# Performance work log

Hardware: AMD Instinct MI355X
Metric: run time of the kernel (lower is better)

The kernel has to match this reference:

```python
import jax, jax.numpy as jnp
import numpy as np

HIDDEN = 768
FFN = 3072
E = 8
TOP_K = 2


def setup_inputs() -> dict:
    key = jax.random.key(0)
    k_x, k_r, k_w1, k_w2 = jax.random.split(key, 4)
    x = jax.random.normal(k_x, (1, 1024, HIDDEN), dtype=jnp.float32)
    # nn.Linear(hidden, E, bias=False): weight applied as x @ W^T; store as [H, E]
    bound = 1.0 / np.sqrt(HIDDEN)
    router_w = jax.random.uniform(k_r, (HIDDEN, E), minval=-bound, maxval=bound, dtype=jnp.float32)
    w1 = jax.random.normal(k_w1, (E, HIDDEN, FFN), dtype=jnp.float32) * 0.02
    w2 = jax.random.normal(k_w2, (E, FFN, HIDDEN), dtype=jnp.float32) * 0.02
    return {"x": x, "router_w": router_w, "w1": w1, "w2": w2}


def reference(x, router_w, w1, w2):
    B, T, H = x.shape
    xf = x.reshape(-1, H)                                  # [N, H]
    logits = xf @ router_w                                 # [N, E] (eval mode: no noise)
    probs = jax.nn.softmax(logits, axis=-1)
    top_v, top_i = jax.lax.top_k(probs, TOP_K)             # [N, K]
    top_v = top_v / jnp.sum(top_v, axis=-1, keepdims=True)  # renormalize top-k probs
    # Combine top-k weights into a dense per-expert gate; zero gates make the
    # dense per-expert computation mathematically identical to sparse dispatch.
    gates = jnp.sum(jax.nn.one_hot(top_i, E, dtype=xf.dtype) * top_v[..., None], axis=1)  # [N, E]
    h = jax.nn.gelu(jnp.einsum('nh,ehf->enf', xf, w1), approximate=False)  # [E, N, F]
    y = jnp.einsum('enf,efh->enh', h, w2)                  # [E, N, H]
    out = jnp.einsum('ne,enh->nh', gates, y)               # [N, H]
    return out.reshape(B, T, H)
```

## Files before the change

kernel.cpp:

```cpp
#include <hip/hip_runtime.h>
#include <cmath>

#define NTOK 1024
#define HD   768
#define FF   3072
#define NE   8
#define NSLOT (NTOK * 2)
#define BK   64
#define CLD  130
#define NB_CONV 4608

typedef unsigned short u16;
typedef unsigned int   u32;
typedef __bf16 bf16x8 __attribute__((ext_vector_type(8)));
typedef float  f32x4  __attribute__((ext_vector_type(4)));
typedef u16    u16x8  __attribute__((ext_vector_type(8)));

__device__ __forceinline__ u16 f2bf(float f) {
  union { float f; u32 u; } v; v.f = f;
  u32 r = v.u + 0x7FFFu + ((v.u >> 16) & 1u);
  return (u16)(r >> 16);
}

__device__ __forceinline__ void load16(const void* g, void* l) {
  __builtin_amdgcn_global_load_lds(
      (const __attribute__((address_space(1))) u32*)g,
      (__attribute__((address_space(3))) u32*)l, 16, 0, 0);
}

__global__ __launch_bounds__(256) void convert_router_kernel(
    const float* __restrict__ w1, const float* __restrict__ w2,
    u16* __restrict__ w1t, u16* __restrict__ w2t,
    const float* __restrict__ x, const float* __restrict__ rw,
    u16* __restrict__ xb, int* __restrict__ counts,
    int* __restrict__ ti, int* __restrict__ tpos, float* __restrict__ tg)
{
  __shared__ char smem[NE * HD * 4];
  const int tid  = threadIdx.x;
  const int lane = tid & 63;
  const int wid  = tid >> 6;

  if (blockIdx.x < NB_CONV) {
    const int z   = blockIdx.x / 288;
    const int rem = blockIdx.x % 288;
    const float* src; u16* dst; int K, N, n0, k0;
    if (z < NE) {
      src = w1 + (size_t)z * HD * FF;  dst = w1t + (size_t)z * FF * HD;
      K = HD; N = FF;
      n0 = (rem % 48) * 64;  k0 = (rem / 48) * 128;
    } else {
      src = w2 + (size_t)(z - NE) * FF * HD;  dst = w2t + (size_t)(z - NE) * HD * FF;
      K = FF; N = HD;
      k0 = (rem % 24) * 128; n0 = (rem / 24) * 64;
    }
    u16* lt = (u16*)smem;
    const int rr = tid >> 4;
    const int cc = (tid & 15) << 2;
#pragma unroll
    for (int j = 0; j < 8; ++j) {
      const int k = j * 16 + rr;
      const float4 v = *(const float4*)(src + (size_t)(k0 + k) * N + n0 + cc);
      lt[(cc + 0) * CLD + k] = f2bf(v.x); lt[(cc + 1) * CLD + k] = f2bf(v.y);
      lt[(cc + 2) * CLD + k] = f2bf(v.z); lt[(cc + 3) * CLD + k] = f2bf(v.w);
    }
    __syncthreads();
    const int l15 = lane & 15;
    const int r4  = lane >> 4;
#pragma unroll
    for (int s = 0; s < 4; ++s) {
      const int r = wid * 16 + s * 4 + r4;
      u16x8 v;
#pragma unroll
      for (int d = 0; d < 8; ++d) v[d] = lt[r * CLD + l15 * 8 + d];
      *(u16x8*)(dst + (size_t)(n0 + r) * K + k0 + l15 * 8) = v;
    }
  } else {
    float* rwt = (float*)smem;
    for (int i = tid; i < NE * HD; i += 256) {
      const int h = i >> 3, e = i & 7;
      rwt[e * HD + h] = rw[i];
    }
    __syncthreads();

    const int t = (blockIdx.x - NB_CONV) * 4 + wid;
    const float* xrow = x + (size_t)t * HD;
    u16* xbrow = xb + (size_t)t * HD;

    float acc[NE] = {};
#pragma unroll
    for (int j = 0; j < 12; ++j) {
      const int h = lane + j * 64;
      const float xv = xrow[h];
      xbrow[h] = f2bf(xv);
#pragma unroll
      for (int e = 0; e < NE; ++e) acc[e] += xv * rwt[e * HD + h];
    }
#pragma unroll
    for (int e = 0; e < NE; ++e) {
      float v = acc[e];
#pragma unroll
      for (int off = 32; off; off >>= 1) v += __shfl_down(v, off, 64);
      acc[e] = v;
    }

    if (lane == 0) {
      float v0 = -1e30f, v1 = -1e30f; int i0 = 0, i1 = 0;
#pragma unroll
      for (int e = 0; e < NE; ++e) {
        const float p = acc[e];
        if (p > v0) { v1 = v0; i1 = i0; v0 = p; i0 = e; }
        else if (p > v1) { v1 = p; i1 = e; }
      }
      const float e1 = expf(v1 - v0);
      const float g0 = 1.0f / (1.0f + e1);
      const float g1 = e1 / (1.0f + e1);
      const int p0 = atomicAdd(&counts[i0], 1);
      const int p1 = atomicAdd(&counts[i1], 1);
      ti[2 * t] = i0;  ti[2 * t + 1] = i1;
      tpos[2 * t] = p0; tpos[2 * t + 1] = p1;
      tg[2 * t] = g0;  tg[2 * t + 1] = g1;
    }
  }
}

__global__ __launch_bounds__(1024) void router_scatter(
    const int* __restrict__ counts, const int* __restrict__ ti,
    const int* __restrict__ tpos, const float* __restrict__ tg,
    int* __restrict__ tos, float* __restrict__ gos, int* __restrict__ seg)
{
  __shared__ int offs[NE];
  const int t = threadIdx.x;
  if (t == 0) {
    int o = 0;
    for (int e = 0; e < NE; ++e) {
      offs[e] = o; seg[e] = o; seg[NE + e] = counts[e]; o += counts[e];
    }
  }
  __syncthreads();
  const int i0 = ti[2 * t], i1 = ti[2 * t + 1];
  const int s0 = offs[i0] + tpos[2 * t];
  const int s1 = offs[i1] + tpos[2 * t + 1];
  tos[s0] = t; gos[s0] = tg[2 * t];
  tos[s1] = t; gos[s1] = tg[2 * t + 1];
}


__global__ __launch_bounds__(256) void ffn1_kernel(
    const u16* __restrict__ xb, const u16* __restrict__ w1t,
    const int* __restrict__ tos, const int* __restrict__ seg,
    u16* __restrict__ hbuf)
{
  const int e   = blockIdx.z;
  const int cnt = seg[NE + e];
  const int m0  = blockIdx.y * 128;
  if (m0 >= cnt) return;
  const int start = seg[e];
  const int n0    = blockIdx.x * 64;

  __shared__ __align__(16) u16 As[128 * 64];
  __shared__ __align__(16) u16 Bs[64 * 64];
  __shared__ int toks[128];

  const int tid = threadIdx.x;
  if (tid < 128) toks[tid] = tos[start + min(m0 + tid, cnt - 1)];
  __syncthreads();

  const int lane = tid & 63;
  const int wid  = tid >> 6;
  const int rsub = lane >> 3;
  const int c8   = (lane & 7) ^ rsub;

  const u16* ag[4]; u16* al[4];
#pragma unroll
  for (int i = 0; i < 4; ++i) {
    const int rb = wid * 8 + i * 32;
    ag[i] = xb + (size_t)toks[rb + rsub] * HD + c8 * 8;
    al[i] = As + rb * 64;
  }
  const u16* bg[2]; u16* bl[2];
#pragma unroll
  for (int i = 0; i < 2; ++i) {
    const int rb = wid * 8 + i * 32;
    bg[i] = w1t + ((size_t)e * FF + n0 + rb + rsub) * HD + c8 * 8;
    bl[i] = Bs + rb * 64;
  }

  const int wm  = (wid >> 1) << 6;
  const int wn  = (wid & 1) << 5;
  const int q   = lane >> 4;
  const int r16 = lane & 15;

  f32x4 acc[4][2] = {};

  for (int k0 = 0; k0 < HD; k0 += BK) {
#pragma unroll
    for (int i = 0; i < 4; ++i) load16(ag[i] + k0, al[i]);
#pragma unroll
    for (int i = 0; i < 2; ++i) load16(bg[i] + k0, bl[i]);
    __syncthreads();
#pragma unroll
    for (int s = 0; s < 2; ++s) {
      const int pa = ((s << 2) + q) ^ (r16 & 7);
      bf16x8 af[4], bf[2];
#pragma unroll
      for (int t = 0; t < 4; ++t)
        af[t] = *(const bf16x8*)(&As[(wm + t * 16 + r16) * 64 + pa * 8]);
#pragma unroll
      for (int t = 0; t < 2; ++t)
        bf[t] = *(const bf16x8*)(&Bs[(wn + t * 16 + r16) * 64 + pa * 8]);
#pragma unroll
      for (int t = 0; t < 4; ++t)
#pragma unroll
        for (int c = 0; c < 2; ++c)
          acc[t][c] = __builtin_amdgcn_mfma_f32_16x16x32_bf16(af[t], bf[c], acc[t][c], 0, 0, 0);
    }
    __syncthreads();
  }

#pragma unroll
  for (int t = 0; t < 4; ++t) {
    const int mbase = m0 + wm + t * 16 + q * 4;
#pragma unroll
    for (int i = 0; i < 4; ++i) {
      if (mbase + i < cnt) {
        u16* drow = hbuf + (size_t)(start + mbase + i) * FF + n0 + wn;
#pragma unroll
        for (int c = 0; c < 2; ++c) {
          float v = acc[t][c][i];
          v = 0.5f * v * (1.0f + erff(v * 0.70710678118f));
          drow[c * 16 + r16] = f2bf(v);
        }
      }
    }
  }
}

#define KSPLIT 4
#define KSEG   (FF / KSPLIT)

__global__ __launch_bounds__(256) void ffn2_kernel(
    const u16* __restrict__ hbuf, const u16* __restrict__ w2t,
    const int* __restrict__ tos, const float* __restrict__ gos,
    const int* __restrict__ seg, float* __restrict__ out)
{
  const int ez  = blockIdx.z;
  const int e   = ez >> 2;
  const int ks  = ez & 3;
  const int cnt = seg[NE + e];
  const int m0  = blockIdx.y * 128;
  if (m0 >= cnt) return;
  const int start = seg[e];
  const int n0    = blockIdx.x * 64;
  const int kbase = ks * KSEG;

  __shared__ __align__(16) u16 As[128 * 64];
  __shared__ __align__(16) u16 Bs[64 * 64];
  __shared__ int   toks[128];
  __shared__ float gates[128];

  const int tid = threadIdx.x;
  if (tid < 128) {
    const int idx = start + min(m0 + tid, cnt - 1);
    toks[tid]  = tos[idx];
    gates[tid] = gos[idx];
  }
  __syncthreads();

  const int lane = tid & 63;
  const int wid  = tid >> 6;
  const int rsub = lane >> 3;
  const int c8   = (lane & 7) ^ rsub;

  const u16* ag[4]; u16* al[4];
#pragma unroll
  for (int i = 0; i < 4; ++i) {
    const int rb = wid * 8 + i * 32;
    ag[i] = hbuf + (size_t)(start + min(m0 + rb + rsub, cnt - 1)) * FF + kbase + c8 * 8;
    al[i] = As + rb * 64;
  }
  const u16* bg[2]; u16* bl[2];
#pragma unroll
  for (int i = 0; i < 2; ++i) {
    const int rb = wid * 8 + i * 32;
    bg[i] = w2t + ((size_t)e * HD + n0 + rb + rsub) * FF + kbase + c8 * 8;
    bl[i] = Bs + rb * 64;
  }

  const int wm  = (wid >> 1) << 6;
  const int wn  = (wid & 1) << 5;
  const int q   = lane >> 4;
  const int r16 = lane & 15;

  f32x4 acc[4][2] = {};

  for (int k0 = 0; k0 < KSEG; k0 += BK) {
#pragma unroll
    for (int i = 0; i < 4; ++i) load16(ag[i] + k0, al[i]);
#pragma unroll
    for (int i = 0; i < 2; ++i) load16(bg[i] + k0, bl[i]);
    __syncthreads();
#pragma unroll
    for (int s = 0; s < 2; ++s) {
      const int pa = ((s << 2) + q) ^ (r16 & 7);
      bf16x8 af[4], bf[2];
#pragma unroll
      for (int t = 0; t < 4; ++t)
        af[t] = *(const bf16x8*)(&As[(wm + t * 16 + r16) * 64 + pa * 8]);
#pragma unroll
      for (int t = 0; t < 2; ++t)
        bf[t] = *(const bf16x8*)(&Bs[(wn + t * 16 + r16) * 64 + pa * 8]);
#pragma unroll
      for (int t = 0; t < 4; ++t)
#pragma unroll
        for (int c = 0; c < 2; ++c)
          acc[t][c] = __builtin_amdgcn_mfma_f32_16x16x32_bf16(af[t], bf[c], acc[t][c], 0, 0, 0);
    }
    __syncthreads();
  }

#pragma unroll
  for (int t = 0; t < 4; ++t) {
    const int mbase = wm + t * 16 + q * 4;
#pragma unroll
    for (int i = 0; i < 4; ++i) {
      const int mloc = mbase + i;
      if (m0 + mloc < cnt) {
        const int tok  = toks[mloc];
        const float g  = gates[mloc];
        float* drow = out + (size_t)tok * HD + n0 + wn;
#pragma unroll
        for (int c = 0; c < 2; ++c) {
          atomicAdd(drow + c * 16 + r16, g * acc[t][c][i]);
        }
      }
    }
  }
}

extern "C" void kernel_launch(void* const* d_in, const int* in_sizes, int n_in,
                              void* d_out, int out_size, void* d_ws, size_t ws_size,
                              hipStream_t stream) {
  const float* x  = (const float*)d_in[0];
  const float* rw = (const float*)d_in[1];
  const float* w1 = (const float*)d_in[2];
  const float* w2 = (const float*)d_in[3];
  float* out = (float*)d_out;

  char* ws = (char*)d_ws;
  const size_t o_xb    = 0;
  const size_t o_hbuf  = o_xb + (size_t)NTOK * HD * 2;
  const size_t o_tos   = o_hbuf + (size_t)NSLOT * FF * 2;
  const size_t o_gos   = o_tos + (size_t)NSLOT * 4;
  const size_t o_seg   = o_gos + (size_t)NSLOT * 4;
  const size_t o_cnt   = o_seg + 64 * 4;
  const size_t o_ti    = o_cnt + NE * 4;
  const size_t o_tpos  = o_ti + (size_t)NSLOT * 4;
  const size_t o_tg    = o_tpos + (size_t)NSLOT * 4;
  const size_t o_w1t   = (o_tg + (size_t)NSLOT * 4 + 255) & ~(size_t)255;
  const size_t o_w2t   = o_w1t + (size_t)NE * HD * FF * 2;
  u16*   xb    = (u16*)(ws + o_xb);
  u16*   hbuf  = (u16*)(ws + o_hbuf);
  int*   tos   = (int*)(ws + o_tos);
  float* gos   = (float*)(ws + o_gos);
  int*   seg   = (int*)(ws + o_seg);
  int*   cnts  = (int*)(ws + o_cnt);
  int*   ti    = (int*)(ws + o_ti);
  int*   tpos  = (int*)(ws + o_tpos);
  float* tg    = (float*)(ws + o_tg);
  u16*   w1t   = (u16*)(ws + o_w1t);
  u16*   w2t   = (u16*)(ws + o_w2t);

  hipMemsetAsync(d_out, 0, (size_t)NTOK * HD * sizeof(float), stream);
  hipMemsetAsync(cnts, 0, NE * sizeof(int), stream);
  hipLaunchKernelGGL(convert_router_kernel, dim3(NB_CONV + NTOK / 4), dim3(256), 0, stream,
                     w1, w2, w1t, w2t, x, rw, xb, cnts, ti, tpos, tg);
  hipLaunchKernelGGL(router_scatter, dim3(1), dim3(1024), 0, stream,
                     cnts, ti, tpos, tg, tos, gos, seg);
  hipLaunchKernelGGL(ffn1_kernel, dim3(FF / 64, NTOK / 128, NE), dim3(256), 0, stream,
                     xb, w1t, tos, seg, hbuf);
  hipLaunchKernelGGL(ffn2_kernel, dim3(HD / 64, NTOK / 128, NE * KSPLIT), dim3(256), 0, stream,
                     hbuf, w2t, tos, gos, seg, out);
}
```

Measured before the change: 271.6 us.

## Double-buffer LDS tiles in expert GEMMs and trim convert kernel shared memory

Both expert GEMM kernels now use two LDS buffers and prefetch the next K tile with global_load_lds while MFMAs run on the current one. This is meant to hide global-load latency behind compute. The convert/router kernel now issues all eight global loads before the LDS writes. It also reads router weights directly from global memory instead of staging a transposed copy in LDS, which cuts its shared memory from 24KB to about 16KB. One hazard: the prefetch into the other buffer may be issued before every wave has left the previous reads of that buffer, and correctness relies on the trailing barrier. The doubled LDS footprint in the GEMMs may also lower occupancy.

```diff
diff --git a/kernel.cpp b/kernel.cpp
--- a/kernel.cpp
+++ b/kernel.cpp
@@ -35,7 +35,7 @@
     u16* __restrict__ xb, int* __restrict__ counts,
     int* __restrict__ ti, int* __restrict__ tpos, float* __restrict__ tg)
 {
-  __shared__ char smem[NE * HD * 4];
+  __shared__ char smem[64 * CLD * 2];
   const int tid  = threadIdx.x;
   const int lane = tid & 63;
   const int wid  = tid >> 6;
@@ -56,32 +56,31 @@
     u16* lt = (u16*)smem;
     const int rr = tid >> 4;
     const int cc = (tid & 15) << 2;
+
+    const float* s0 = src + (size_t)(k0 + rr) * N + n0 + cc;
+    float4 v[8];
+#pragma unroll
+    for (int j = 0; j < 8; ++j) v[j] = *(const float4*)(s0 + (size_t)j * 16 * N);
+
 #pragma unroll
     for (int j = 0; j < 8; ++j) {
       const int k = j * 16 + rr;
-      const float4 v = *(const float4*)(src + (size_t)(k0 + k) * N + n0 + cc);
-      lt[(cc + 0) * CLD + k] = f2bf(v.x); lt[(cc + 1) * CLD + k] = f2bf(v.y);
-      lt[(cc + 2) * CLD + k] = f2bf(v.z); lt[(cc + 3) * CLD + k] = f2bf(v.w);
+      lt[(cc + 0) * CLD + k] = f2bf(v[j].x); lt[(cc + 1) * CLD + k] = f2bf(v[j].y);
+      lt[(cc + 2) * CLD + k] = f2bf(v[j].z); lt[(cc + 3) * CLD + k] = f2bf(v[j].w);
     }
     __syncthreads();
+
     const int l15 = lane & 15;
     const int r4  = lane >> 4;
 #pragma unroll
     for (int s = 0; s < 4; ++s) {
       const int r = wid * 16 + s * 4 + r4;
-      u16x8 v;
-#pragma unroll
-      for (int d = 0; d < 8; ++d) v[d] = lt[r * CLD + l15 * 8 + d];
-      *(u16x8*)(dst + (size_t)(n0 + r) * K + k0 + l15 * 8) = v;
+      u16x8 vv;
+#pragma unroll
+      for (int d = 0; d < 8; ++d) vv[d] = lt[r * CLD + l15 * 8 + d];
+      *(u16x8*)(dst + (size_t)(n0 + r) * K + k0 + l15 * 8) = vv;
     }
   } else {
-    float* rwt = (float*)smem;
-    for (int i = tid; i < NE * HD; i += 256) {
-      const int h = i >> 3, e = i & 7;
-      rwt[e * HD + h] = rw[i];
-    }
-    __syncthreads();
-
     const int t = (blockIdx.x - NB_CONV) * 4 + wid;
     const float* xrow = x + (size_t)t * HD;
     u16* xbrow = xb + (size_t)t * HD;
@@ -92,8 +91,12 @@
       const int h = lane + j * 64;
       const float xv = xrow[h];
       xbrow[h] = f2bf(xv);
-#pragma unroll
-      for (int e = 0; e < NE; ++e) acc[e] += xv * rwt[e * HD + h];
+      const float4 r0 = *(const float4*)(rw + h * 8);
+      const float4 r1 = *(const float4*)(rw + h * 8 + 4);
+      acc[0] += xv * r0.x; acc[1] += xv * r0.y;
+      acc[2] += xv * r0.z; acc[3] += xv * r0.w;
+      acc[4] += xv * r1.x; acc[5] += xv * r1.y;
+      acc[6] += xv * r1.z; acc[7] += xv * r1.w;
     }
 #pragma unroll
     for (int e = 0; e < NE; ++e) {
@@ -157,8 +160,8 @@
   const int start = seg[e];
   const int n0    = blockIdx.x * 64;
 
-  __shared__ __align__(16) u16 As[128 * 64];
-  __shared__ __align__(16) u16 Bs[64 * 64];
+  __shared__ __align__(16) u16 As[2][128 * 64];
+  __shared__ __align__(16) u16 Bs[2][64 * 64];
   __shared__ int toks[128];
 
   const int tid = threadIdx.x;
@@ -170,19 +173,19 @@
   const int rsub = lane >> 3;
   const int c8   = (lane & 7) ^ rsub;
 
-  const u16* ag[4]; u16* al[4];
+  const u16* ag[4]; int ao[4];
 #pragma unroll
   for (int i = 0; i < 4; ++i) {
     const int rb = wid * 8 + i * 32;
     ag[i] = xb + (size_t)toks[rb + rsub] * HD + c8 * 8;
-    al[i] = As + rb * 64;
-  }
-  const u16* bg[2]; u16* bl[2];
+    ao[i] = rb * 64;
+  }
+  const u16* bg[2]; int bo[2];
 #pragma unroll
   for (int i = 0; i < 2; ++i) {
     const int rb = wid * 8 + i * 32;
     bg[i] = w1t + ((size_t)e * FF + n0 + rb + rsub) * HD + c8 * 8;
-    bl[i] = Bs + rb * 64;
+    bo[i] = rb * 64;
   }
 
   const int wm  = (wid >> 1) << 6;
@@ -192,22 +195,31 @@
 
   f32x4 acc[4][2] = {};
 
+#pragma unroll
+  for (int i = 0; i < 4; ++i) load16(ag[i], &As[0][ao[i]]);
+#pragma unroll
+  for (int i = 0; i < 2; ++i) load16(bg[i], &Bs[0][bo[i]]);
+  __syncthreads();
+
+  int cur = 0;
   for (int k0 = 0; k0 < HD; k0 += BK) {
-#pragma unroll
-    for (int i = 0; i < 4; ++i) load16(ag[i] + k0, al[i]);
-#pragma unroll
-    for (int i = 0; i < 2; ++i) load16(bg[i] + k0, bl[i]);
-    __syncthreads();
+    const int nxt = cur ^ 1;
+    if (k0 + BK < HD) {
+#pragma unroll
+      for (int i = 0; i < 4; ++i) load16(ag[i] + k0 + BK, &As[nxt][ao[i]]);
+#pragma unroll
+      for (int i = 0; i < 2; ++i) load16(bg[i] + k0 + BK, &Bs[nxt][bo[i]]);
+    }
 #pragma unroll
     for (int s = 0; s < 2; ++s) {
       const int pa = ((s << 2) + q) ^ (r16 & 7);
       bf16x8 af[4], bf[2];
 #pragma unroll
       for (int t = 0; t < 4; ++t)
-        af[t] = *(const bf16x8*)(&As[(wm + t * 16 + r16) * 64 + pa * 8]);
+        af[t] = *(const bf16x8*)(&As[cur][(wm + t * 16 + r16) * 64 + pa * 8]);
 #pragma unroll
       for (int t = 0; t < 2; ++t)
-        bf[t] = *(const bf16x8*)(&Bs[(wn + t * 16 + r16) * 64 + pa * 8]);
+        bf[t] = *(const bf16x8*)(&Bs[cur][(wn + t * 16 + r16) * 64 + pa * 8]);
 #pragma unroll
       for (int t = 0; t < 4; ++t)
 #pragma unroll
@@ -215,6 +227,7 @@
           acc[t][c] = __builtin_amdgcn_mfma_f32_16x16x32_bf16(af[t], bf[c], acc[t][c], 0, 0, 0);
     }
     __syncthreads();
+    cur = nxt;
   }
 
 #pragma unroll
@@ -253,8 +266,8 @@
   const int n0    = blockIdx.x * 64;
   const int kbase = ks * KSEG;
 
-  __shared__ __align__(16) u16 As[128 * 64];
-  __shared__ __align__(16) u16 Bs[64 * 64];
+  __shared__ __align__(16) u16 As[2][128 * 64];
+  __shared__ __align__(16) u16 Bs[2][64 * 64];
   __shared__ int   toks[128];
   __shared__ float gates[128];
 
@@ -271,19 +284,19 @@
   const int rsub = lane >> 3;
   const int c8   = (lane & 7) ^ rsub;
 
-  const u16* ag[4]; u16* al[4];
+  const u16* ag[4]; int ao[4];
 #pragma unroll
   for (int i = 0; i < 4; ++i) {
     const int rb = wid * 8 + i * 32;
     ag[i] = hbuf + (size_t)(start + min(m0 + rb + rsub, cnt - 1)) * FF + kbase + c8 * 8;
-    al[i] = As + rb * 64;
-  }
-  const u16* bg[2]; u16* bl[2];
+    ao[i] = rb * 64;
+  }
+  const u16* bg[2]; int bo[2];
 #pragma unroll
   for (int i = 0; i < 2; ++i) {
     const int rb = wid * 8 + i * 32;
     bg[i] = w2t + ((size_t)e * HD + n0 + rb + rsub) * FF + kbase + c8 * 8;
-    bl[i] = Bs + rb * 64;
+    bo[i] = rb * 64;
   }
 
   const int wm  = (wid >> 1) << 6;
@@ -293,22 +306,31 @@
 
   f32x4 acc[4][2] = {};
 
+#pragma unroll
+  for (int i = 0; i < 4; ++i) load16(ag[i], &As[0][ao[i]]);
+#pragma unroll
+  for (int i = 0; i < 2; ++i) load16(bg[i], &Bs[0][bo[i]]);
+  __syncthreads();
+
+  int cur = 0;
   for (int k0 = 0; k0 < KSEG; k0 += BK) {
-#pragma unroll
-    for (int i = 0; i < 4; ++i) load16(ag[i] + k0, al[i]);
-#pragma unroll
-    for (int i = 0; i < 2; ++i) load16(bg[i] + k0, bl[i]);
-    __syncthreads();
+    const int nxt = cur ^ 1;
+    if (k0 + BK < KSEG) {
+#pragma unroll
+      for (int i = 0; i < 4; ++i) load16(ag[i] + k0 + BK, &As[nxt][ao[i]]);
+#pragma unroll
+      for (int i = 0; i < 2; ++i) load16(bg[i] + k0 + BK, &Bs[nxt][bo[i]]);
+    }
 #pragma unroll
     for (int s = 0; s < 2; ++s) {
       const int pa = ((s << 2) + q) ^ (r16 & 7);
       bf16x8 af[4], bf[2];
 #pragma unroll
       for (int t = 0; t < 4; ++t)
-        af[t] = *(const bf16x8*)(&As[(wm + t * 16 + r16) * 64 + pa * 8]);
+        af[t] = *(const bf16x8*)(&As[cur][(wm + t * 16 + r16) * 64 + pa * 8]);
 #pragma unroll
       for (int t = 0; t < 2; ++t)
-        bf[t] = *(const bf16x8*)(&Bs[(wn + t * 16 + r16) * 64 + pa * 8]);
+        bf[t] = *(const bf16x8*)(&Bs[cur][(wn + t * 16 + r16) * 64 + pa * 8]);
 #pragma unroll
       for (int t = 0; t < 4; ++t)
 #pragma unroll
@@ -316,6 +338,7 @@
           acc[t][c] = __builtin_amdgcn_mfma_f32_16x16x32_bf16(af[t], bf[c], acc[t][c], 0, 0, 0);
     }
     __syncthreads();
+    cur = nxt;
   }
 
 #pragma unroll
```

Result: no change. 275.0 us (+1.3%).

## Overlap w2 bf16 conversion with ffn1 GEMM in one fused launch

Applied to the files above, without the earlier changes.

Splits weight conversion so only w1 is converted alongside the router, while w2 conversion tiles are interleaved (3 of every 7 blocks) with ffn1 GEMM tiles in a single combined kernel. The memory-bound conversion of w2 can then overlap with the compute-bound first FFN GEMM. The router now reads router weights directly as float4 instead of first staging a transposed copy in LDS, which shrinks shared memory. The conversion loads are batched ahead of the LDS writes. The combined kernel uses a larger shared buffer, which may reduce occupancy for the GEMM blocks.

```diff
diff --git a/kernel.cpp b/kernel.cpp
--- a/kernel.cpp
+++ b/kernel.cpp
@@ -8,7 +8,11 @@
 #define NSLOT (NTOK * 2)
 #define BK   64
 #define CLD  130
-#define NB_CONV 4608
+
+#define NB_ROUTER 256
+#define NB_CONV1  2304
+#define NB_CONV2  2304
+#define NB_FFN1   3072
 
 typedef unsigned short u16;
 typedef unsigned int   u32;
@@ -28,61 +32,59 @@
       (__attribute__((address_space(3))) u32*)l, 16, 0, 0);
 }
 
-__global__ __launch_bounds__(256) void convert_router_kernel(
-    const float* __restrict__ w1, const float* __restrict__ w2,
-    u16* __restrict__ w1t, u16* __restrict__ w2t,
+__device__ __forceinline__ void conv_tile(
+    const float* __restrict__ src, u16* __restrict__ dst,
+    int K, int N, int k0, int n0, char* smem, int tid, int lane, int wid)
+{
+  u16* lt = (u16*)smem;
+  const int rr = tid >> 4;
+  const int cc = (tid & 15) << 2;
+
+  const float* s0 = src + (size_t)(k0 + rr) * N + n0 + cc;
+  float4 v[8];
+#pragma unroll
+  for (int j = 0; j < 8; ++j) v[j] = *(const float4*)(s0 + (size_t)j * 16 * N);
+  __builtin_amdgcn_sched_barrier(0);
+
+#pragma unroll
+  for (int j = 0; j < 8; ++j) {
+    const int k = j * 16 + rr;
+    lt[(cc + 0) * CLD + k] = f2bf(v[j].x); lt[(cc + 1) * CLD + k] = f2bf(v[j].y);
+    lt[(cc + 2) * CLD + k] = f2bf(v[j].z); lt[(cc + 3) * CLD + k] = f2bf(v[j].w);
+  }
+  __syncthreads();
+
+  const int l15 = lane & 15;
+  const int r4  = lane >> 4;
+#pragma unroll
+  for (int s = 0; s < 4; ++s) {
+    const int r = wid * 16 + s * 4 + r4;
+    u16x8 vv;
+#pragma unroll
+    for (int d = 0; d < 8; ++d) vv[d] = lt[r * CLD + l15 * 8 + d];
+    *(u16x8*)(dst + (size_t)(n0 + r) * K + k0 + l15 * 8) = vv;
+  }
+}
+
+__global__ __launch_bounds__(256, 4) void conv1_router_kernel(
+    const float* __restrict__ w1, u16* __restrict__ w1t,
     const float* __restrict__ x, const float* __restrict__ rw,
     u16* __restrict__ xb, int* __restrict__ counts,
     int* __restrict__ ti, int* __restrict__ tpos, float* __restrict__ tg)
 {
-  __shared__ char smem[NE * HD * 4];
+  __shared__ __align__(16) char smem[64 * CLD * 2];
   const int tid  = threadIdx.x;
   const int lane = tid & 63;
   const int wid  = tid >> 6;
 
-  if (blockIdx.x < NB_CONV) {
-    const int z   = blockIdx.x / 288;
-    const int rem = blockIdx.x % 288;
-    const float* src; u16* dst; int K, N, n0, k0;
-    if (z < NE) {
-      src = w1 + (size_t)z * HD * FF;  dst = w1t + (size_t)z * FF * HD;
-      K = HD; N = FF;
-      n0 = (rem % 48) * 64;  k0 = (rem / 48) * 128;
-    } else {
-      src = w2 + (size_t)(z - NE) * FF * HD;  dst = w2t + (size_t)(z - NE) * HD * FF;
-      K = FF; N = HD;
-      k0 = (rem % 24) * 128; n0 = (rem / 24) * 64;
-    }
-    u16* lt = (u16*)smem;
-    const int rr = tid >> 4;
-    const int cc = (tid & 15) << 2;
-#pragma unroll
-    for (int j = 0; j < 8; ++j) {
-      const int k = j * 16 + rr;
-      const float4 v = *(const float4*)(src + (size_t)(k0 + k) * N + n0 + cc);
-      lt[(cc + 0) * CLD + k] = f2bf(v.x); lt[(cc + 1) * CLD + k] = f2bf(v.y);
-      lt[(cc + 2) * CLD + k] = f2bf(v.z); lt[(cc + 3) * CLD + k] = f2bf(v.w);
-    }
-    __syncthreads();
-    const int l15 = lane & 15;
-    const int r4  = lane >> 4;
-#pragma unroll
-    for (int s = 0; s < 4; ++s) {
-      const int r = wid * 16 + s * 4 + r4;
-      u16x8 v;
-#pragma unroll
-      for (int d = 0; d < 8; ++d) v[d] = lt[r * CLD + l15 * 8 + d];
-      *(u16x8*)(dst + (size_t)(n0 + r) * K + k0 + l15 * 8) = v;
-    }
+  if (blockIdx.x >= NB_ROUTER) {
+    const int cid = blockIdx.x - NB_ROUTER;
+    const int z   = cid / 288;
+    const int rem = cid % 288;
+    conv_tile(w1 + (size_t)z * HD * FF, w1t + (size_t)z * FF * HD,
+              HD, FF, (rem / 48) * 128, (rem % 48) * 64, smem, tid, lane, wid);
   } else {
-    float* rwt = (float*)smem;
-    for (int i = tid; i < NE * HD; i += 256) {
-      const int h = i >> 3, e = i & 7;
-      rwt[e * HD + h] = rw[i];
-    }
-    __syncthreads();
-
-    const int t = (blockIdx.x - NB_CONV) * 4 + wid;
+    const int t = blockIdx.x * 4 + wid;
     const float* xrow = x + (size_t)t * HD;
     u16* xbrow = xb + (size_t)t * HD;
 
@@ -92,8 +94,12 @@
       const int h = lane + j * 64;
       const float xv = xrow[h];
       xbrow[h] = f2bf(xv);
-#pragma unroll
-      for (int e = 0; e < NE; ++e) acc[e] += xv * rwt[e * HD + h];
+      const float4 r0 = *(const float4*)(rw + h * 8);
+      const float4 r1 = *(const float4*)(rw + h * 8 + 4);
+      acc[0] += xv * r0.x; acc[1] += xv * r0.y;
+      acc[2] += xv * r0.z; acc[3] += xv * r0.w;
+      acc[4] += xv * r1.x; acc[5] += xv * r1.y;
+      acc[6] += xv * r1.z; acc[7] += xv * r1.w;
     }
 #pragma unroll
     for (int e = 0; e < NE; ++e) {
@@ -144,29 +150,44 @@
   tos[s1] = t; gos[s1] = tg[2 * t + 1];
 }
 
-
-__global__ __launch_bounds__(256) void ffn1_kernel(
+__global__ __launch_bounds__(256) void ffn1_conv2_kernel(
     const u16* __restrict__ xb, const u16* __restrict__ w1t,
     const int* __restrict__ tos, const int* __restrict__ seg,
-    u16* __restrict__ hbuf)
+    u16* __restrict__ hbuf,
+    const float* __restrict__ w2, u16* __restrict__ w2t)
 {
-  const int e   = blockIdx.z;
+  __shared__ __align__(16) char smem[25088];
+  const int tid  = threadIdx.x;
+  const int lane = tid & 63;
+  const int wid  = tid >> 6;
+
+  const int g  = blockIdx.x / 7;
+  const int r7 = blockIdx.x % 7;
+
+  if (r7 >= 4) {
+    const int cid = g * 3 + (r7 - 4);
+    const int z   = cid / 288;
+    const int rem = cid % 288;
+    conv_tile(w2 + (size_t)z * FF * HD, w2t + (size_t)z * HD * FF,
+              FF, HD, (rem % 24) * 128, (rem / 24) * 64, smem, tid, lane, wid);
+    return;
+  }
+
+  const int fid = g * 4 + r7;
+  const int e   = fid / 384;
+  const int m0  = ((fid / 48) % 8) * 128;
+  const int n0  = (fid % 48) * 64;
   const int cnt = seg[NE + e];
-  const int m0  = blockIdx.y * 128;
   if (m0 >= cnt) return;
   const int start = seg[e];
-  const int n0    = blockIdx.x * 64;
-
-  __shared__ __align__(16) u16 As[128 * 64];
-  __shared__ __align__(16) u16 Bs[64 * 64];
-  __shared__ int toks[128];
-
-  const int tid = threadIdx.x;
+
+  u16* As   = (u16*)smem;
+  u16* Bs   = (u16*)(smem + 16384);
+  int* toks = (int*)(smem + 24576);
+
   if (tid < 128) toks[tid] = tos[start + min(m0 + tid, cnt - 1)];
   __syncthreads();
 
-  const int lane = tid & 63;
-  const int wid  = tid >> 6;
   const int rsub = lane >> 3;
   const int c8   = (lane & 7) ^ rsub;
 
@@ -372,12 +393,12 @@
 
   hipMemsetAsync(d_out, 0, (size_t)NTOK * HD * sizeof(float), stream);
   hipMemsetAsync(cnts, 0, NE * sizeof(int), stream);
-  hipLaunchKernelGGL(convert_router_kernel, dim3(NB_CONV + NTOK / 4), dim3(256), 0, stream,
-                     w1, w2, w1t, w2t, x, rw, xb, cnts, ti, tpos, tg);
+  hipLaunchKernelGGL(conv1_router_kernel, dim3(NB_ROUTER + NB_CONV1), dim3(256), 0, stream,
+                     w1, w1t, x, rw, xb, cnts, ti, tpos, tg);
   hipLaunchKernelGGL(router_scatter, dim3(1), dim3(1024), 0, stream,
                      cnts, ti, tpos, tg, tos, gos, seg);
-  hipLaunchKernelGGL(ffn1_kernel, dim3(FF / 64, NTOK / 128, NE), dim3(256), 0, stream,
-                     xb, w1t, tos, seg, hbuf);
+  hipLaunchKernelGGL(ffn1_conv2_kernel, dim3((NB_FFN1 + NB_CONV2)), dim3(256), 0, stream,
+                     xb, w1t, tos, seg, hbuf, w2, w2t);
   hipLaunchKernelGGL(ffn2_kernel, dim3(HD / 64, NTOK / 128, NE * KSPLIT), dim3(256), 0, stream,
                      hbuf, w2t, tos, gos, seg, out);
 }
```

New measurement: 273.4 us. No clear change (+0.7%).
